# Kernel optimization log

Measured on AMD Instinct MI355X. Metric: run time of the kernel, lower is better.

The kernel has to match this reference:

```python
import jax, jax.numpy as jnp
import numpy as np

N = 50000          # nodes
E = 1_600_000      # edges (avg degree 32)
F_IN = 48          # node features (df columns 1:-1)
H, C = 8, 8        # conv1: 8 heads x 8 channels
NC = 2             # num_classes
NEG_SLOPE = 0.2    # PyG GATConv default leaky_relu slope


def setup_inputs() -> dict:
    key = jax.random.key(0)
    ks = jax.random.split(key, 9)
    s = 0.1
    return {
        "x": jax.random.normal(ks[0], (N, F_IN), jnp.float32),
        "edge_index": jax.random.randint(ks[1], (2, E), 0, N, dtype=jnp.int64),
        "W1": jax.random.normal(ks[2], (F_IN, H * C), jnp.float32) * s,
        "att_src1": jax.random.normal(ks[3], (H, C), jnp.float32) * s,
        "att_dst1": jax.random.normal(ks[4], (H, C), jnp.float32) * s,
        "b1": jnp.zeros((H * C,), jnp.float32),
        "W2": jax.random.normal(ks[5], (H * C, NC), jnp.float32) * s,
        "att_src2": jax.random.normal(ks[6], (1, NC), jnp.float32) * s,
        "att_dst2": jax.random.normal(ks[7], (1, NC), jnp.float32) * s,
        "b2": jnp.zeros((NC,), jnp.float32),
    }


def _gat_conv(x, src, dst, W, a_src, a_dst, b, heads, out_ch, concat):
    """PyG GATConv: linear -> per-edge leaky_relu attention -> segment softmax
    over destination nodes -> scatter-sum aggregation."""
    n = x.shape[0]
    h = (x @ W).reshape(n, heads, out_ch)               # [N, H, C]
    e_src = (h * a_src).sum(-1)                          # [N, H]
    e_dst = (h * a_dst).sum(-1)                          # [N, H]
    e = jax.nn.leaky_relu(e_src[src] + e_dst[dst], NEG_SLOPE)  # [E, H]
    # numerically stable segment softmax over incoming edges of each dst node
    m = jax.ops.segment_max(e, dst, num_segments=n)      # [N, H]
    ex = jnp.exp(e - m[dst])
    den = jax.ops.segment_sum(ex, dst, num_segments=n)   # [N, H]
    alpha = ex / den[dst]                                # [E, H]
    out = jax.ops.segment_sum(h[src] * alpha[:, :, None], dst, num_segments=n)
    out = out.reshape(n, heads * out_ch) if concat else out.mean(axis=1)
    return out + b


def reference(x, edge_index, W1, att_src1, att_dst1, b1, W2, att_src2, att_dst2, b2):
    n = x.shape[0]
    loop = jnp.arange(n, dtype=edge_index.dtype)  # GATConv add_self_loops=True
    src = jnp.concatenate([edge_index[0], loop])
    dst = jnp.concatenate([edge_index[1], loop])
    h = _gat_conv(x, src, dst, W1, att_src1, att_dst1, b1, H, C, True)
    h = jax.nn.elu(h)
    out = _gat_conv(h, src, dst, W2, att_src2, att_dst2, b2, 1, NC, False)
    return jax.nn.log_softmax(out, axis=1)
```

## Files before the change

### kernel.cpp

```cpp
#include <hip/hip_runtime.h>
#include <hip/hip_bf16.h>
#include <math.h>

#define NN 50000
#define FIN 48
#define HC 64
#define NHEAD 8
#define NCH 8
#define NCLS 2
#define NEG 0.2f
#define LOG2E 1.44269504f

#define NPB 98
#define NBKT 512
#define CAP 4096
#define BCHUNK 4096

__global__ void k_zero(int* p, int n) {
    int i = blockIdx.x * blockDim.x + threadIdx.x;
    if (i < n) p[i] = 0;
}


__global__ void k_bin_h1(const int* __restrict__ ei, int* __restrict__ bcur,
                         int* __restrict__ pairs, int e, int tot, int nbin,
                         const float* __restrict__ x, const float* __restrict__ W1,
                         const float* __restrict__ as1, const float* __restrict__ ad1,
                         __hip_bfloat16* __restrict__ h1b, __hip_bfloat16* __restrict__ es1b,
                         float* __restrict__ ed1, int n) {
    __shared__ int hist[NBKT];
    __shared__ int gbase[NBKT];
    __shared__ float xs[16][FIN];
    int t = threadIdx.x;
    if ((int)blockIdx.x < nbin) {
        hist[t] = 0; hist[t + 256] = 0;
        __syncthreads();
        int base = blockIdx.x * BCHUNK;
        int end = min(base + BCHUNK, tot);
        for (int i = base + t; i < end; i += 256) {
            int d = (i < e) ? ei[e + i] : (i - e);
            atomicAdd(&hist[d / NPB], 1);
        }
        __syncthreads();
        for (int u = t; u < NBKT; u += 256) {
            int h = hist[u];
            gbase[u] = h ? atomicAdd(&bcur[u], h) : 0;
        }
        __syncthreads();
        hist[t] = 0; hist[t + 256] = 0;
        __syncthreads();
        for (int i = base + t; i < end; i += 256) {
            int s, d;
            if (i < e) { s = ei[i]; d = ei[e + i]; }
            else       { s = d = i - e; }
            int b = d / NPB;
            int p = gbase[b] + atomicAdd(&hist[b], 1);
            if (p < CAP) pairs[b * CAP + p] = ((d - b * NPB) << 16) | s;
        }
    } else {
        int j = t & 63, row = t >> 6;
        float wreg[FIN];
        #pragma unroll
        for (int k = 0; k < FIN; ++k) wreg[k] = W1[k * HC + j];
        float asl = as1[j] * LOG2E, adl = ad1[j] * LOG2E;
        int hh = j >> 3, c = j & 7;
        int ngroups = (n + 15) >> 4;
        int GB = gridDim.x - nbin;
        for (int g = blockIdx.x - nbin; g < ngroups; g += GB) {
            int nb = g * 16;
            __syncthreads();
            for (int i = t; i < 16 * FIN; i += 256) {
                int l = i / FIN, k = i % FIN;
                int nd = nb + l;
                xs[l][k] = (nd < n) ? x[nd * FIN + k] : 0.f;
            }
            __syncthreads();
            #pragma unroll
            for (int m = 0; m < 4; ++m) {
                int l = (row << 2) + m;
                float acc = 0.f;
                #pragma unroll
                for (int k = 0; k < FIN; ++k) acc += xs[l][k] * wreg[k];
                int nd = nb + l;
                if (nd < n) h1b[nd * HC + j] = __float2bfloat16(acc);
                float es = acc * asl, ed = acc * adl;
                es += __shfl_xor(es, 1, 64); es += __shfl_xor(es, 2, 64); es += __shfl_xor(es, 4, 64);
                ed += __shfl_xor(ed, 1, 64); ed += __shfl_xor(ed, 2, 64); ed += __shfl_xor(ed, 4, 64);
                if (nd < n) {
                    if (c == 0) es1b[nd * NHEAD + hh] = __float2bfloat16(es);
                    if (c == 1) ed1[nd * NHEAD + hh] = ed;
                }
            }
        }
    }
}


__global__ void k_bucket_csr(const int* __restrict__ pairs, const int* __restrict__ bcur,
                             int* __restrict__ rowptr, int* __restrict__ degv,
                             int* __restrict__ csr, int n) {
    __shared__ int hist[256];
    int b = blockIdx.x, t = threadIdx.x;
    int lo = b * NPB;
    int nn = min(NPB, n - lo);
    if (nn <= 0) return;
    int base = b * CAP;
    int cnt = min(bcur[b], CAP);
    hist[t] = 0;
    __syncthreads();
    for (int i = t; i < cnt; i += 256) {
        atomicAdd(&hist[pairs[base + i] >> 16], 1);
    }
    __syncthreads();
    int v = hist[t];
    for (int off = 1; off < 256; off <<= 1) {
        int y = (t >= off) ? hist[t - off] : 0;
        __syncthreads();
        hist[t] += y;
        __syncthreads();
    }
    int excl = hist[t] - v;
    if (t < nn) { rowptr[lo + t] = base + excl; degv[lo + t] = v; }
    __syncthreads();
    hist[t] = excl;
    __syncthreads();
    for (int i = t; i < cnt; i += 256) {
        int p = pairs[base + i];
        int pos = atomicAdd(&hist[p >> 16], 1);
        csr[base + pos] = p & 0xFFFF;
    }
}


__global__ void k_agg1(const __hip_bfloat16* __restrict__ h1b, const __hip_bfloat16* __restrict__ es1b,
                       const float* __restrict__ ed1, const int* __restrict__ rowptr,
                       const int* __restrict__ degv, const int* __restrict__ csr,
                       const float* __restrict__ b1,
                       const float* __restrict__ W2, const float* __restrict__ as2,
                       const float* __restrict__ ad2, float4* __restrict__ node2, int n) {
    int wid = (blockIdx.x * blockDim.x + threadIdx.x) >> 6;
    if (wid >= n) return;
    int lane = threadIdx.x & 63;
    int j  = lane >> 3;
    int hw = lane & 7;
    int e4 = lane >> 4;
    int r  = lane & 15;
    int ha = r >> 1;
    int ch0 = (ha << 3) + ((r & 1) << 2);
    int wbase = (e4 << 3) + ha;
    int start = rowptr[wid];
    int cnt = degv[wid];
    float edv = ed1[wid * NHEAD + hw];
    float sumw = 0.f;
    float a0 = 0.f, a1 = 0.f, a2 = 0.f, a3 = 0.f;
    int nbatch = cnt >> 3;

    int rv = csr[start + min(lane, cnt - 1)];

    int sl; float ev; uint2 va, vb;
    if (nbatch > 0) {
        sl = __shfl(rv, j, 64);
        ev = __bfloat162float(es1b[sl * NHEAD + hw]);
        int su0 = __shfl(sl, e4 << 3, 64);
        int su1 = __shfl(sl, (4 + e4) << 3, 64);
        va = *(const uint2*)(h1b + su0 * HC + ch0);
        vb = *(const uint2*)(h1b + su1 * HC + ch0);
        for (int b = 1; b < nbatch; ++b) {
            int sl_n;
            if (b < 8) sl_n = __shfl(rv, (b << 3) + j, 64);
            else       sl_n = csr[start + (b << 3) + j];
            float ev_n = __bfloat162float(es1b[sl_n * NHEAD + hw]);
            int su0n = __shfl(sl_n, e4 << 3, 64);
            int su1n = __shfl(sl_n, (4 + e4) << 3, 64);
            uint2 va_n = *(const uint2*)(h1b + su0n * HC + ch0);
            uint2 vb_n = *(const uint2*)(h1b + su1n * HC + ch0);
            float tt = ev + edv;
            tt = fmaxf(tt, NEG * tt);
            float w = exp2f(tt);
            sumw += w;
            float wj0 = __shfl(w, wbase, 64);
            float wj1 = __shfl(w, wbase + 32, 64);
            a0 += wj0 * __uint_as_float(va.x << 16);
            a1 += wj0 * __uint_as_float(va.x & 0xffff0000u);
            a2 += wj0 * __uint_as_float(va.y << 16);
            a3 += wj0 * __uint_as_float(va.y & 0xffff0000u);
            a0 += wj1 * __uint_as_float(vb.x << 16);
            a1 += wj1 * __uint_as_float(vb.x & 0xffff0000u);
            a2 += wj1 * __uint_as_float(vb.y << 16);
            a3 += wj1 * __uint_as_float(vb.y & 0xffff0000u);
            sl = sl_n; ev = ev_n; va = va_n; vb = vb_n;
        }
        float tt = ev + edv;
        tt = fmaxf(tt, NEG * tt);
        float w = exp2f(tt);
        sumw += w;
        float wj0 = __shfl(w, wbase, 64);
        float wj1 = __shfl(w, wbase + 32, 64);
        a0 += wj0 * __uint_as_float(va.x << 16);
        a1 += wj0 * __uint_as_float(va.x & 0xffff0000u);
        a2 += wj0 * __uint_as_float(va.y << 16);
        a3 += wj0 * __uint_as_float(va.y & 0xffff0000u);
        a0 += wj1 * __uint_as_float(vb.x << 16);
        a1 += wj1 * __uint_as_float(vb.x & 0xffff0000u);
        a2 += wj1 * __uint_as_float(vb.y << 16);
        a3 += wj1 * __uint_as_float(vb.y & 0xffff0000u);
    }
    int i = nbatch << 3;
    if (i < cnt) {
        int idx = min(i + j, cnt - 1);
        int slt = (cnt <= 64) ? __shfl(rv, idx, 64) : csr[start + idx];
        float evt = __bfloat162float(es1b[slt * NHEAD + hw]) + edv;
        evt = fmaxf(evt, NEG * evt);
        float w = (i + j < cnt) ? exp2f(evt) : 0.f;
        sumw += w;
        #pragma unroll
        for (int it = 0; it < 2; ++it) {
            int su   = __shfl(slt, ((it << 2) + e4) << 3, 64);
            float wj = __shfl(w, wbase + (it << 5), 64);
            uint2 v = *(const uint2*)(h1b + su * HC + ch0);
            a0 += wj * __uint_as_float(v.x << 16);
            a1 += wj * __uint_as_float(v.x & 0xffff0000u);
            a2 += wj * __uint_as_float(v.y << 16);
            a3 += wj * __uint_as_float(v.y & 0xffff0000u);
        }
    }
    sumw += __shfl_xor(sumw, 8, 64);
    sumw += __shfl_xor(sumw, 16, 64);
    sumw += __shfl_xor(sumw, 32, 64);
    a0 += __shfl_xor(a0, 16, 64); a0 += __shfl_xor(a0, 32, 64);
    a1 += __shfl_xor(a1, 16, 64); a1 += __shfl_xor(a1, 32, 64);
    a2 += __shfl_xor(a2, 16, 64); a2 += __shfl_xor(a2, 32, 64);
    a3 += __shfl_xor(a3, 16, 64); a3 += __shfl_xor(a3, 32, 64);
    float sden = __shfl(sumw, ha, 64);
    float4 bv = *(const float4*)(b1 + ch0);
    float o0 = a0 / sden + bv.x;
    float o1 = a1 / sden + bv.y;
    float o2 = a2 / sden + bv.z;
    float o3 = a3 / sden + bv.w;
    o0 = o0 > 0.f ? o0 : expm1f(o0);
    o1 = o1 > 0.f ? o1 : expm1f(o1);
    o2 = o2 > 0.f ? o2 : expm1f(o2);
    o3 = o3 > 0.f ? o3 : expm1f(o3);
    float4 w01 = *(const float4*)(W2 + ch0 * 2);
    float4 w23 = *(const float4*)(W2 + ch0 * 2 + 4);
    float p0 = o0 * w01.x + o1 * w01.z + o2 * w23.x + o3 * w23.z;
    float p1 = o0 * w01.y + o1 * w01.w + o2 * w23.y + o3 * w23.w;
    #pragma unroll
    for (int off = 8; off > 0; off >>= 1) {
        p0 += __shfl_xor(p0, off, 64);
        p1 += __shfl_xor(p1, off, 64);
    }
    if (lane == 0) {
        float es2v = (p0 * as2[0] + p1 * as2[1]) * LOG2E;
        float ed2v = (p0 * ad2[0] + p1 * ad2[1]) * LOG2E;
        node2[wid] = make_float4(es2v, p0, p1, ed2v);
    }
}


__global__ void k_agg2(const float4* __restrict__ node2, const int* __restrict__ rowptr,
                       const int* __restrict__ degv, const int* __restrict__ csr,
                       const float* __restrict__ b2, float* __restrict__ out, int n) {
    int lane = threadIdx.x & 63;
    int wid = ((blockIdx.x * blockDim.x + threadIdx.x) >> 6) * 4 + (lane >> 4);
    if (wid >= n) return;
    int l16 = lane & 15;
    int start = rowptr[wid];
    int cnt = degv[wid];
    float edv = ((const float*)node2)[wid * 4 + 3];
    float sw = 0.f, a0 = 0.f, a1 = 0.f;
    for (int i = l16; i < cnt; i += 16) {
        int s = __builtin_nontemporal_load(csr + start + i);
        float4 t = node2[s];
        float val = t.x + edv;
        val = fmaxf(val, NEG * val);
        float w = exp2f(val);
        sw += w;
        a0 += w * t.y;
        a1 += w * t.z;
    }
    #pragma unroll
    for (int off = 8; off > 0; off >>= 1) {
        sw += __shfl_xor(sw, off, 16);
        a0 += __shfl_xor(a0, off, 16);
        a1 += __shfl_xor(a1, off, 16);
    }
    if (l16 == 0) {
        float z0 = a0 / sw + b2[0];
        float z1 = a1 / sw + b2[1];
        float mz = fmaxf(z0, z1);
        float lse = mz + logf(__expf(z0 - mz) + __expf(z1 - mz));
        out[wid * NCLS + 0] = z0 - lse;
        out[wid * NCLS + 1] = z1 - lse;
    }
}


extern "C" void kernel_launch(void* const* d_in, const int* in_sizes, int n_in,
                              void* d_out, int out_size, void* d_ws, size_t ws_size,
                              hipStream_t stream) {
    const float* x   = (const float*)d_in[0];
    const int*   ei  = (const int*)d_in[1];
    const float* W1  = (const float*)d_in[2];
    const float* as1 = (const float*)d_in[3];
    const float* ad1 = (const float*)d_in[4];
    const float* b1  = (const float*)d_in[5];
    const float* W2  = (const float*)d_in[6];
    const float* as2 = (const float*)d_in[7];
    const float* ad2 = (const float*)d_in[8];
    const float* b2  = (const float*)d_in[9];
    float* out = (float*)d_out;

    const int n = in_sizes[0] / FIN;
    const int e = in_sizes[1] / 2;
    const int tot = e + n;

    char* ws = (char*)d_ws;
    size_t off = 0;
    auto alloc = [&](size_t bytes) -> void* {
        void* p = ws + off;
        off += (bytes + 255) & ~(size_t)255;
        return p;
    };
    __hip_bfloat16* h1b  = (__hip_bfloat16*)alloc((size_t)n * HC * 2);
    __hip_bfloat16* es1b = (__hip_bfloat16*)alloc((size_t)n * NHEAD * 2);
    int* pairs   = (int*)alloc((size_t)NBKT * CAP * 4);
    int* csr     = (int*)alloc((size_t)NBKT * CAP * 4);
    float* ed1   = (float*)alloc((size_t)n * NHEAD * 4);
    float4* node2 = (float4*)alloc((size_t)n * 16);
    int* rowptr  = (int*)alloc((size_t)n * 4);
    int* degv    = (int*)alloc((size_t)n * 4);
    int* bcur    = (int*)alloc((size_t)NBKT * 4);

    const int nbin = (tot + BCHUNK - 1) / BCHUNK;

    k_zero<<<(NBKT + 255) / 256, 256, 0, stream>>>(bcur, NBKT);
    k_bin_h1<<<nbin + 1024, 256, 0, stream>>>(ei, bcur, pairs, e, tot, nbin,
                                              x, W1, as1, ad1, h1b, es1b, ed1, n);
    k_bucket_csr<<<NBKT, 256, 0, stream>>>(pairs, bcur, rowptr, degv, csr, n);
    k_agg1<<<(n * 64 + 255) / 256, 256, 0, stream>>>(h1b, es1b, ed1, rowptr, degv, csr,
                                                     b1, W2, as2, ad2, node2, n);
    k_agg2<<<(n * 16 + 255) / 256, 256, 0, stream>>>(node2, rowptr, degv, csr, b2, out, n);
}
```

Before: 106.5 us.

## Replace global-atomic edge bucketing with per-bin fixed slots and counts

Edge binning now works in one pass. Each thread keeps up to 16 edges in registers, takes a slot from a shared-memory histogram, and writes each edge into a fixed 32-entry region for its (bucket, bin) pair. A per-bin count table is written alongside. This removes the global atomic reservation of bucket space, the second pass over the edge list and the separate zeroing kernel. Self-loops are no longer binned; the CSR build inserts them directly. In exchange, the CSR build must scan a sparse slot array of nbin*32 entries per bucket. Any (bucket, bin) pair with more than 32 edges silently loses edges, so correctness depends on the destinations being spread fairly uniformly.

```diff
diff --git a/kernel.cpp b/kernel.cpp
--- a/kernel.cpp
+++ b/kernel.cpp
@@ -15,47 +15,48 @@
 #define NBKT 512
 #define CAP 4096
 #define BCHUNK 4096
-
-__global__ void k_zero(int* p, int n) {
-    int i = blockIdx.x * blockDim.x + threadIdx.x;
-    if (i < n) p[i] = 0;
-}
-
-
-__global__ void k_bin_h1(const int* __restrict__ ei, int* __restrict__ bcur,
-                         int* __restrict__ pairs, int e, int tot, int nbin,
-                         const float* __restrict__ x, const float* __restrict__ W1,
-                         const float* __restrict__ as1, const float* __restrict__ ad1,
-                         __hip_bfloat16* __restrict__ h1b, __hip_bfloat16* __restrict__ es1b,
-                         float* __restrict__ ed1, int n) {
+#define SLOT 32
+
+
+__global__ __launch_bounds__(256, 4)
+void k_bin_h1(const int* __restrict__ ei, int* __restrict__ cnt,
+              int* __restrict__ pairs, int e, int nbin,
+              const float* __restrict__ x, const float* __restrict__ W1,
+              const float* __restrict__ as1, const float* __restrict__ ad1,
+              __hip_bfloat16* __restrict__ h1b, __hip_bfloat16* __restrict__ es1b,
+              float* __restrict__ ed1, int n) {
     __shared__ int hist[NBKT];
-    __shared__ int gbase[NBKT];
     __shared__ float xs[16][FIN];
     int t = threadIdx.x;
     if ((int)blockIdx.x < nbin) {
+        int bid = blockIdx.x;
         hist[t] = 0; hist[t + 256] = 0;
         __syncthreads();
-        int base = blockIdx.x * BCHUNK;
-        int end = min(base + BCHUNK, tot);
-        for (int i = base + t; i < end; i += 256) {
-            int d = (i < e) ? ei[e + i] : (i - e);
-            atomicAdd(&hist[d / NPB], 1);
+        int base = bid * BCHUNK;
+        int end = min(base + BCHUNK, e);
+        int pk[16];
+        int bp[16];
+        #pragma unroll
+        for (int k = 0; k < 16; ++k) {
+            int i = base + t + k * 256;
+            if (i < end) {
+                int s = ei[i], d = ei[e + i];
+                int b = d / NPB;
+                int p = atomicAdd(&hist[b], 1);
+                pk[k] = ((d - b * NPB) << 16) | s;
+                bp[k] = (b << 16) | p;
+            } else bp[k] = -1;
         }
         __syncthreads();
-        for (int u = t; u < NBKT; u += 256) {
-            int h = hist[u];
-            gbase[u] = h ? atomicAdd(&bcur[u], h) : 0;
-        }
-        __syncthreads();
-        hist[t] = 0; hist[t + 256] = 0;
-        __syncthreads();
-        for (int i = base + t; i < end; i += 256) {
-            int s, d;
-            if (i < e) { s = ei[i]; d = ei[e + i]; }
-            else       { s = d = i - e; }
-            int b = d / NPB;
-            int p = gbase[b] + atomicAdd(&hist[b], 1);
-            if (p < CAP) pairs[b * CAP + p] = ((d - b * NPB) << 16) | s;
+        cnt[bid * NBKT + t]       = hist[t];
+        cnt[bid * NBKT + t + 256] = hist[t + 256];
+        #pragma unroll
+        for (int k = 0; k < 16; ++k) {
+            if (bp[k] >= 0) {
+                int b = bp[k] >> 16;
+                int p = bp[k] & 0xFFFF;
+                if (p < SLOT) pairs[(b * nbin + bid) * SLOT + p] = pk[k];
+            }
         }
     } else {
         int j = t & 63, row = t >> 6;
@@ -96,20 +97,24 @@
 }
 
 
-__global__ void k_bucket_csr(const int* __restrict__ pairs, const int* __restrict__ bcur,
+__global__ void k_bucket_csr(const int* __restrict__ pairs, const int* __restrict__ cnt,
                              int* __restrict__ rowptr, int* __restrict__ degv,
-                             int* __restrict__ csr, int n) {
+                             int* __restrict__ csr, int n, int nbin) {
+    __shared__ int cnts[512];
     __shared__ int hist[256];
-    int b = blockIdx.x, t = threadIdx.x;
-    int lo = b * NPB;
+    int k = blockIdx.x, t = threadIdx.x;
+    int lo = k * NPB;
     int nn = min(NPB, n - lo);
     if (nn <= 0) return;
-    int base = b * CAP;
-    int cnt = min(bcur[b], CAP);
-    hist[t] = 0;
-    __syncthreads();
-    for (int i = t; i < cnt; i += 256) {
-        atomicAdd(&hist[pairs[base + i] >> 16], 1);
+    for (int b = t; b < nbin; b += 256) cnts[b] = cnt[b * NBKT + k];
+    hist[t] = (t < nn) ? 1 : 0;
+    __syncthreads();
+    int rbase = k * nbin * SLOT;
+    int total_slots = nbin * SLOT;
+    for (int i = t; i < total_slots; i += 256) {
+        if ((i & (SLOT - 1)) < cnts[i >> 5]) {
+            atomicAdd(&hist[pairs[rbase + i] >> 16], 1);
+        }
     }
     __syncthreads();
     int v = hist[t];
@@ -120,14 +125,22 @@
         __syncthreads();
     }
     int excl = hist[t] - v;
+    int base = k * CAP;
     if (t < nn) { rowptr[lo + t] = base + excl; degv[lo + t] = v; }
     __syncthreads();
     hist[t] = excl;
     __syncthreads();
-    for (int i = t; i < cnt; i += 256) {
-        int p = pairs[base + i];
-        int pos = atomicAdd(&hist[p >> 16], 1);
-        csr[base + pos] = p & 0xFFFF;
+    if (t < nn) {
+        csr[base + excl] = lo + t;
+        hist[t] = excl + 1;
+    }
+    __syncthreads();
+    for (int i = t; i < total_slots; i += 256) {
+        if ((i & (SLOT - 1)) < cnts[i >> 5]) {
+            int p = pairs[rbase + i];
+            int pos = atomicAdd(&hist[p >> 16], 1);
+            csr[base + pos] = p & 0xFFFF;
+        }
     }
 }
 
@@ -313,7 +326,7 @@
 
     const int n = in_sizes[0] / FIN;
     const int e = in_sizes[1] / 2;
-    const int tot = e + n;
+    const int nbin = (e + BCHUNK - 1) / BCHUNK;
 
     char* ws = (char*)d_ws;
     size_t off = 0;
@@ -324,20 +337,17 @@
     };
     __hip_bfloat16* h1b  = (__hip_bfloat16*)alloc((size_t)n * HC * 2);
     __hip_bfloat16* es1b = (__hip_bfloat16*)alloc((size_t)n * NHEAD * 2);
-    int* pairs   = (int*)alloc((size_t)NBKT * CAP * 4);
+    int* pairs   = (int*)alloc((size_t)NBKT * nbin * SLOT * 4);
+    int* cnt     = (int*)alloc((size_t)nbin * NBKT * 4);
     int* csr     = (int*)alloc((size_t)NBKT * CAP * 4);
     float* ed1   = (float*)alloc((size_t)n * NHEAD * 4);
     float4* node2 = (float4*)alloc((size_t)n * 16);
     int* rowptr  = (int*)alloc((size_t)n * 4);
     int* degv    = (int*)alloc((size_t)n * 4);
-    int* bcur    = (int*)alloc((size_t)NBKT * 4);
-
-    const int nbin = (tot + BCHUNK - 1) / BCHUNK;
-
-    k_zero<<<(NBKT + 255) / 256, 256, 0, stream>>>(bcur, NBKT);
-    k_bin_h1<<<nbin + 1024, 256, 0, stream>>>(ei, bcur, pairs, e, tot, nbin,
+
+    k_bin_h1<<<nbin + 1024, 256, 0, stream>>>(ei, cnt, pairs, e, nbin,
                                               x, W1, as1, ad1, h1b, es1b, ed1, n);
-    k_bucket_csr<<<NBKT, 256, 0, stream>>>(pairs, bcur, rowptr, degv, csr, n);
+    k_bucket_csr<<<NBKT, 256, 0, stream>>>(pairs, cnt, rowptr, degv, csr, n, nbin);
     k_agg1<<<(n * 64 + 255) / 256, 256, 0, stream>>>(h1b, es1b, ed1, rowptr, degv, csr,
                                                      b1, W2, as2, ad2, node2, n);
     k_agg2<<<(n * 16 + 255) / 256, 256, 0, stream>>>(node2, rowptr, degv, csr, b2, out, n);
```

Result: slower. 120.2 us (+12.8%).
